# Kernel optimization log

Hardware: AMD Instinct MI355X
Metric: run time of the kernel (lower is better)

## Reference

```python
import jax, jax.numpy as jnp
import numpy as np

B, N, D, H = 8, 2048, 128, 4
DH = D // H
EPS_LN = 1e-5


def setup_inputs() -> dict:
    key = jax.random.key(0)
    ks = jax.random.split(key, 9)
    x = jax.random.normal(ks[0], (B, N, D), dtype=jnp.float32)
    u = jax.random.uniform(ks[1], (N, N), dtype=jnp.float32)
    adj = jnp.where(u > 0.5, u, 0.0)
    adj = adj.at[jnp.arange(N), jnp.arange(N)].set(1.0)
    W = jax.random.normal(ks[2], (D, D), dtype=jnp.float32) * (1.0 / np.sqrt(D))
    a_src = jax.random.normal(ks[3], (H, DH), dtype=jnp.float32) * 0.02
    a_dst = jax.random.normal(ks[4], (H, DH), dtype=jnp.float32) * 0.02
    Wo = jax.random.normal(ks[5], (D, D), dtype=jnp.float32) * (1.0 / np.sqrt(D))
    bo = jnp.zeros((D,), dtype=jnp.float32)
    gamma = jnp.ones((D,), dtype=jnp.float32)
    beta = jnp.zeros((D,), dtype=jnp.float32)
    return {"x": x, "adj_static": adj, "W": W, "a_src": a_src, "a_dst": a_dst,
            "Wo": Wo, "bo": bo, "gamma": gamma, "beta": beta}


def reference(x, adj_static, W, a_src, a_dst, Wo, bo, gamma, beta):
    # h: (B, H, N, DH)
    h = (x @ W.T).reshape(B, N, H, DH).transpose(0, 2, 1, 3)
    src = jnp.einsum('bhnd,hd->bhn', h, a_src)  # (B, H, N)
    dst = jnp.einsum('bhnd,hd->bhn', h, a_dst)  # (B, H, N)
    e = jax.nn.leaky_relu(src[..., :, None] + dst[..., None, :], 0.2)  # (B,H,N,N)
    logA = jnp.log(jnp.clip(adj_static, 1e-8))[None, None]
    mask = (adj_static > 0)[None, None]
    e = jnp.where(mask, e + logA, -jnp.inf)
    attn = jax.nn.softmax(e, axis=-1)  # dropout is identity in eval mode
    out = attn @ h  # (B, H, N, DH)
    out = out.transpose(0, 2, 1, 3).reshape(B, N, D)
    out = out @ Wo.T + bo
    y = x + out
    mu = jnp.mean(y, axis=-1, keepdims=True)
    var = jnp.mean(jnp.square(y - mu), axis=-1, keepdims=True)
    return (y - mu) * jax.lax.rsqrt(var + EPS_LN) * gamma + beta
```

## Files before the change

### kernel.cpp

```cpp
#include <hip/hip_runtime.h>

typedef short bf16x8 __attribute__((ext_vector_type(8)));
typedef float f32x4  __attribute__((ext_vector_type(4)));
typedef float f32x2  __attribute__((ext_vector_type(2)));
typedef int   i32x4  __attribute__((ext_vector_type(4)));
typedef unsigned int u32x2 __attribute__((ext_vector_type(2)));

#define DEV static __device__ __forceinline__
#define LOG2E 1.4426950408889634f

DEV float bfu_to_f(unsigned short s) { return __builtin_bit_cast(float, (unsigned int)s << 16); }
DEV unsigned short f_to_bf(float f) {
  unsigned int u = __builtin_bit_cast(unsigned int, f);
  u += 0x7fffu + ((u >> 16) & 1u);
  return (unsigned short)(u >> 16);
}
DEV unsigned int pack_bf_rne(float lo, float hi) {
  return (unsigned int)f_to_bf(lo) | ((unsigned int)f_to_bf(hi) << 16);
}
DEV float fplo(int u) { return __builtin_bit_cast(float, (unsigned int)u << 16); }
DEV float fphi(int u) { return __builtin_bit_cast(float, (unsigned int)u & 0xffff0000u); }
DEV float nexp2(float x) {
#if __has_builtin(__builtin_amdgcn_exp2f)
  return __builtin_amdgcn_exp2f(x);
#else
  return exp2f(x);
#endif
}
template<bool HI> DEV unsigned int pk_fp8(float a, float b, unsigned int old) {
  return __builtin_amdgcn_cvt_pk_fp8_f32(a, b, old, HI);
}
template<int W> DEV f32x2 upk_fp8(unsigned int w) {
  auto r = __builtin_amdgcn_cvt_pk_f32_fp8(w, W);
  f32x2 o; o[0] = r[0]; o[1] = r[1]; return o;
}

DEV bool detect_f32(const void* adj) { return ((const float*)adj)[0] == 1.0f; }

template<bool F32> DEV float ldS(const void* p, size_t i) {
  if constexpr (F32) return ((const float*)p)[i];
  else               return bfu_to_f(((const unsigned short*)p)[i]);
}
template<bool F32> DEV void ld8f(const void* p, size_t i, float* o) {
  if constexpr (F32) {
    const float* f = (const float*)p + i;
    f32x4 a = *(const f32x4*)f, b = *(const f32x4*)(f + 4);
    o[0]=a[0]; o[1]=a[1]; o[2]=a[2]; o[3]=a[3];
    o[4]=b[0]; o[5]=b[1]; o[6]=b[2]; o[7]=b[3];
  } else {
    i32x4 w = *(const i32x4*)((const unsigned short*)p + i);
#pragma unroll
    for (int k = 0; k < 4; ++k) {
      unsigned int u = (unsigned int)w[k];
      o[2*k]   = __builtin_bit_cast(float, u << 16);
      o[2*k+1] = __builtin_bit_cast(float, u & 0xffff0000u);
    }
  }
}
template<bool F32> DEV bf16x8 ldfrag(const void* p, size_t i) {
  if constexpr (F32) {
    float o[8]; ld8f<true>(p, i, o);
    union { bf16x8 v; unsigned short u[8]; } r;
#pragma unroll
    for (int k = 0; k < 8; ++k) r.u[k] = f_to_bf(o[k]);
    return r.v;
  } else {
    return __builtin_bit_cast(bf16x8, *(const i32x4*)((const unsigned short*)p + i));
  }
}

__global__ __launch_bounds__(256) void k_prep(const void* __restrict__ adj,
                                              unsigned char* __restrict__ adjf) {
  const size_t i0 = ((size_t)blockIdx.x * 256 + threadIdx.x) * 8;
  u32x2 o;
  if (detect_f32(adj)) {
    const float* a = (const float*)adj + i0;
    f32x4 v0 = *(const f32x4*)a, v1 = *(const f32x4*)(a + 4);
    o[0] = pk_fp8<true>(v0[2], v0[3], pk_fp8<false>(v0[0], v0[1], 0u));
    o[1] = pk_fp8<true>(v1[2], v1[3], pk_fp8<false>(v1[0], v1[1], 0u));
  } else {
    i32x4 w = *(const i32x4*)((const unsigned short*)adj + i0);
    float f[8];
#pragma unroll
    for (int k = 0; k < 4; ++k) {
      unsigned int u = (unsigned int)w[k];
      f[2*k]   = __builtin_bit_cast(float, u << 16);
      f[2*k+1] = __builtin_bit_cast(float, u & 0xffff0000u);
    }
    o[0] = pk_fp8<true>(f[2], f[3], pk_fp8<false>(f[0], f[1], 0u));
    o[1] = pk_fp8<true>(f[6], f[7], pk_fp8<false>(f[4], f[5], 0u));
  }
  *(u32x2*)(adjf + i0) = o;
}

template<bool F32> DEV void k_h_body(const void* __restrict__ x, const void* __restrict__ W,
                                     unsigned char* __restrict__ hT,
                                     unsigned short (&t_s)[16][136]) {
  const int tid = threadIdx.x, lane = tid & 63, wave = tid >> 6;
  const int nt = blockIdx.x >> 3, ct = blockIdx.x & 7;
  const int m = lane & 15, q = lane >> 4;
  bf16x8 wf[4];
#pragma unroll
  for (int k = 0; k < 4; ++k)
    wf[k] = ldfrag<F32>(W, (size_t)(ct * 16 + m) * 128 + q * 8 + k * 32);
#pragma unroll
  for (int s = 0; s < 2; ++s) {
    const int nsub = wave * 2 + s;
    const size_t xr = (size_t)(nt * 128 + nsub * 16 + m) * 128 + q * 8;
    f32x4 acc = {0.f, 0.f, 0.f, 0.f};
#pragma unroll
    for (int k = 0; k < 4; ++k)
      acc = __builtin_amdgcn_mfma_f32_16x16x32_bf16(ldfrag<F32>(x, xr + k * 32), wf[k],
                                                    acc, 0, 0, 0);
    u32x2 w2; w2[0] = pack_bf_rne(acc[0], acc[1]); w2[1] = pack_bf_rne(acc[2], acc[3]);
    *(u32x2*)&t_s[m][nsub * 16 + q * 4] = w2;
  }
  __syncthreads();
  const int row = tid >> 4, c8 = tid & 15;
  const int chg = ct * 16 + row, hh = chg >> 5, dloc = chg & 31;
  const int ng = nt * 128 + c8 * 8, b = ng >> 11, nl = ng & 2047;
  i32x4 v = *(const i32x4*)&t_s[row][c8 * 8];
  float f[8];
#pragma unroll
  for (int k = 0; k < 4; ++k) {
    unsigned int u = (unsigned int)v[k];
    f[2*k]   = __builtin_bit_cast(float, u << 16);
    f[2*k+1] = __builtin_bit_cast(float, u & 0xffff0000u);
  }
  u32x2 o;
  o[0] = pk_fp8<true>(f[2], f[3], pk_fp8<false>(f[0], f[1], 0u));
  o[1] = pk_fp8<true>(f[6], f[7], pk_fp8<false>(f[4], f[5], 0u));
  *(u32x2*)(hT + ((size_t)((b * 4 + hh) * 32 + dloc)) * 2048 + nl) = o;
}
__global__ __launch_bounds__(256) void k_h(const void* x, const void* W,
                                           unsigned char* hT, const void* adj) {
  __shared__ __align__(16) unsigned short t_s[16][136];
  if (detect_f32(adj)) k_h_body<true>(x, W, hT, t_s); else k_h_body<false>(x, W, hT, t_s);
}

template<bool F32> DEV void k_sd_body(const unsigned char* __restrict__ hT,
                                      const void* __restrict__ a_src, const void* __restrict__ a_dst,
                                      float* __restrict__ rv, unsigned int* __restrict__ fhv) {
  const int t = blockIdx.x * 256 + threadIdx.x;
  const int n = t & 2047, bh = t >> 11, hh = bh & 3;
  const unsigned char* col = hT + (size_t)bh * 32 * 2048 + n;
  float s = 0.f, d = 0.f;
#pragma unroll
  for (int dd = 0; dd < 32; ++dd) {
    const float v = __builtin_amdgcn_cvt_f32_fp8((int)col[(size_t)dd * 2048], 0);
    s += v * ldS<F32>(a_src, hh * 32 + dd);
    d += v * ldS<F32>(a_dst, hh * 32 + dd);
  }
  rv[t] = nexp2(-0.8f * LOG2E * s);
  const float F = nexp2(LOG2E * d);
  const float H = nexp2(0.2f * LOG2E * d);
  fhv[t] = pack_bf_rne(F, H);
}
__global__ __launch_bounds__(256) void k_sd(const unsigned char* hT, const void* a_src,
                                            const void* a_dst, float* rv, unsigned int* fhv,
                                            const void* adj) {
  if (detect_f32(adj)) k_sd_body<true>(hT, a_src, a_dst, rv, fhv);
  else                 k_sd_body<false>(hT, a_src, a_dst, rv, fhv);
}

struct SmemAttn {
  unsigned char adj[2][64][136];
  unsigned char vt[2][32][136];
  unsigned int  fh[2][128];
};

__global__ __launch_bounds__(256, 4) void k_attn(const unsigned char* __restrict__ adjf,
                                                 const unsigned char* __restrict__ hT,
                                                 const float* __restrict__ rv,
                                                 const unsigned int* __restrict__ fhv,
                                                 unsigned short* __restrict__ ao) {
  __shared__ __align__(16) SmemAttn sm;
  const int tid = threadIdx.x, lane = tid & 63, wave = tid >> 6;
  const int bh = blockIdx.x & 31, iblk = blockIdx.x >> 5;
  const int b = bh >> 2, hh = bh & 3;
  const int m = lane & 15, q = lane >> 4;
  const int i0 = iblk * 64;
  const int jqb = wave * 32 + q * 8;

  const int ar = tid >> 2, ac = (tid & 3) * 32;
  const int vr = tid >> 3, vc = (tid & 7) * 16;
  const bool fstg = tid < 32;

  const unsigned char* ap = adjf + (size_t)(i0 + ar) * 2048 + ac;
  const unsigned char* vp = hT + ((size_t)bh * 32 + vr) * 2048 + vc;
  const unsigned int*  fp = fhv + (size_t)bh * 2048 + tid * 4;

  i32x4 arr0, arr1, vrr, frr;

  arr0 = *(const i32x4*)(ap);
  arr1 = *(const i32x4*)(ap + 16);
  vrr  = *(const i32x4*)vp;
  if (fstg) frr = *(const i32x4*)fp;
  *(i32x4*)&sm.adj[0][ar][ac]      = arr0;
  *(i32x4*)&sm.adj[0][ar][ac + 16] = arr1;
  *(i32x4*)&sm.vt[0][vr][vc] = vrr;
  if (fstg) *(i32x4*)&sm.fh[0][tid * 4] = frr;
  __syncthreads();

  float Riv[4];
#pragma unroll
  for (int it = 0; it < 4; ++it)
    Riv[it] = rv[bh * 2048 + i0 + it * 16 + m];

  f32x4 accA[4], accB[4], accD[4];
#pragma unroll
  for (int it = 0; it < 4; ++it) {
    accA[it] = f32x4{0.f,0.f,0.f,0.f};
    accB[it] = f32x4{0.f,0.f,0.f,0.f};
    accD[it] = f32x4{0.f,0.f,0.f,0.f};
  }
  const long Aones = 0x3838383838383838L;

#pragma unroll 2
  for (int c = 0; c < 16; ++c) {
    const int cb = c & 1;
    if (c < 15) {
      const int o = (c + 1) * 128;
      arr0 = *(const i32x4*)(ap + o);
      arr1 = *(const i32x4*)(ap + o + 16);
      vrr  = *(const i32x4*)(vp + o);
      if (fstg) frr = *(const i32x4*)(fp + o);
    }
    const long A0 = *(const long*)&sm.vt[cb][m][jqb];
    const long A1 = *(const long*)&sm.vt[cb][16 + m][jqb];
    const i32x4 u0 = *(const i32x4*)&sm.fh[cb][jqb];
    const i32x4 u1 = *(const i32x4*)&sm.fh[cb][jqb + 4];
    f32x2 F0 = {fplo(u0[0]), fplo(u0[1])}, H0 = {fphi(u0[0]), fphi(u0[1])};
    f32x2 F1 = {fplo(u0[2]), fplo(u0[3])}, H1 = {fphi(u0[2]), fphi(u0[3])};
    f32x2 F2 = {fplo(u1[0]), fplo(u1[1])}, H2 = {fphi(u1[0]), fphi(u1[1])};
    f32x2 F3 = {fplo(u1[2]), fplo(u1[3])}, H3 = {fphi(u1[2]), fphi(u1[3])};
#pragma unroll
    for (int it = 0; it < 4; ++it) {
      const int il = it * 16 + m;
      const u32x2 aw = *(const u32x2*)&sm.adj[cb][il][jqb];
      f32x2 av0 = upk_fp8<0>(aw[0]), av1 = upk_fp8<1>(aw[0]);
      f32x2 av2 = upk_fp8<0>(aw[1]), av3 = upk_fp8<1>(aw[1]);
      const f32x2 Ri2 = {Riv[it], Riv[it]};
      f32x2 w0 = __builtin_elementwise_max(F0, Ri2 * H0);
      f32x2 w1 = __builtin_elementwise_max(F1, Ri2 * H1);
      f32x2 w2 = __builtin_elementwise_max(F2, Ri2 * H2);
      f32x2 w3 = __builtin_elementwise_max(F3, Ri2 * H3);
      f32x2 pv0 = av0 * w0, pv1 = av1 * w1, pv2 = av2 * w2, pv3 = av3 * w3;
      u32x2 bp;
      bp[0] = pk_fp8<true>(pv1[0], pv1[1], pk_fp8<false>(pv0[0], pv0[1], 0u));
      bp[1] = pk_fp8<true>(pv3[0], pv3[1], pk_fp8<false>(pv2[0], pv2[1], 0u));
      const long B = __builtin_bit_cast(long, bp);
      accA[it] = __builtin_amdgcn_mfma_f32_16x16x32_fp8_fp8(A0,    B, accA[it], 0, 0, 0);
      accB[it] = __builtin_amdgcn_mfma_f32_16x16x32_fp8_fp8(A1,    B, accB[it], 0, 0, 0);
      accD[it] = __builtin_amdgcn_mfma_f32_16x16x32_fp8_fp8(Aones, B, accD[it], 0, 0, 0);
    }
    if (c < 15) {
      const int nb = cb ^ 1;
      *(i32x4*)&sm.adj[nb][ar][ac]      = arr0;
      *(i32x4*)&sm.adj[nb][ar][ac + 16] = arr1;
      *(i32x4*)&sm.vt[nb][vr][vc] = vrr;
      if (fstg) *(i32x4*)&sm.fh[nb][tid * 4] = frr;
    }
    __syncthreads();
  }

  float* red = (float*)&sm;
  if (wave == 1 || wave == 3) {
    const int reg = (wave >> 1) * 3072;
#pragma unroll
    for (int it = 0; it < 4; ++it) {
      const int base = reg + (it * 64 + lane) * 12;
      *(f32x4*)&red[base]     = accA[it];
      *(f32x4*)&red[base + 4] = accB[it];
      red[base + 8] = accD[it][0];
    }
  }
  __syncthreads();
  if (wave == 0 || wave == 2) {
    const int reg = (wave >> 1) * 3072;
#pragma unroll
    for (int it = 0; it < 4; ++it) {
      const int base = reg + (it * 64 + lane) * 12;
      accA[it] += *(const f32x4*)&red[base];
      accB[it] += *(const f32x4*)&red[base + 4];
      accD[it][0] += red[base + 8];
    }
  }
  __syncthreads();
  if (wave == 2) {
#pragma unroll
    for (int it = 0; it < 4; ++it) {
      const int base = (it * 64 + lane) * 12;
      *(f32x4*)&red[base]     = accA[it];
      *(f32x4*)&red[base + 4] = accB[it];
      red[base + 8] = accD[it][0];
    }
  }
  __syncthreads();
  if (wave == 0) {
#pragma unroll
    for (int it = 0; it < 4; ++it) {
      const int base = (it * 64 + lane) * 12;
      const f32x4 a0 = accA[it] + *(const f32x4*)&red[base];
      const f32x4 a1 = accB[it] + *(const f32x4*)&red[base + 4];
      const float den = accD[it][0] + red[base + 8];
      const float inv = 1.f / fmaxf(den, 1e-20f);
      const int il = it * 16 + m;
      unsigned short* op = ao + ((size_t)(b * 2048) + i0 + il) * 128 + hh * 32 + q * 4;
      u32x2 w0, w1;
      w0[0] = pack_bf_rne(a0[0] * inv, a0[1] * inv);
      w0[1] = pack_bf_rne(a0[2] * inv, a0[3] * inv);
      w1[0] = pack_bf_rne(a1[0] * inv, a1[1] * inv);
      w1[1] = pack_bf_rne(a1[2] * inv, a1[3] * inv);
      *(u32x2*)op        = w0;
      *(u32x2*)(op + 16) = w1;
    }
  }
}

template<bool F32> DEV void k_out_body(const unsigned short* __restrict__ ao,
                                       const void* __restrict__ Wo, const void* __restrict__ bo,
                                       const void* __restrict__ x, const void* __restrict__ gamma,
                                       const void* __restrict__ beta, void* __restrict__ out,
                                       float (&y_s)[16][132]) {
  const int tid = threadIdx.x, lane = tid & 63, wave = tid >> 6;
  const int m = lane & 15, q = lane >> 4;
  const int rbase = blockIdx.x * 16;
  bf16x8 af[4];
#pragma unroll
  for (int k = 0; k < 4; ++k)
    af[k] = ldfrag<false>(ao, ((size_t)(rbase + m)) * 128 + q * 8 + k * 32);
  f32x4 acc[2] = {{0.f,0.f,0.f,0.f},{0.f,0.f,0.f,0.f}};
#pragma unroll
  for (int ct = 0; ct < 2; ++ct) {
    const size_t wrow = (size_t)(wave * 32 + ct * 16 + m) * 128 + q * 8;
#pragma unroll
    for (int k = 0; k < 4; ++k)
      acc[ct] = __builtin_amdgcn_mfma_f32_16x16x32_bf16(af[k], ldfrag<F32>(Wo, wrow + k * 32),
                                                        acc[ct], 0, 0, 0);
  }
#pragma unroll
  for (int ct = 0; ct < 2; ++ct) {
    const int c = wave * 32 + ct * 16 + m;
    const float bov = ldS<F32>(bo, c);
#pragma unroll
    for (int r = 0; r < 4; ++r) {
      const int row = q * 4 + r;
      y_s[row][c] = acc[ct][r] + bov + ldS<F32>(x, (size_t)(rbase + row) * 128 + c);
    }
  }
  __syncthreads();
  const int r = tid >> 4, c16 = tid & 15;
  float vals[8], sum = 0.f, sq = 0.f;
#pragma unroll
  for (int k = 0; k < 8; ++k) {
    const float v = y_s[r][c16 * 8 + k];
    vals[k] = v; sum += v; sq += v * v;
  }
#pragma unroll
  for (int msk = 1; msk < 16; msk <<= 1) {
    sum += __shfl_xor(sum, msk, 16);
    sq  += __shfl_xor(sq,  msk, 16);
  }
  const float mu  = sum * (1.f / 128.f);
  const float var = fmaxf(sq * (1.f / 128.f) - mu * mu, 0.f);
  const float rstd = rsqrtf(var + 1e-5f);
  float o[8];
#pragma unroll
  for (int k = 0; k < 8; ++k) {
    const int c = c16 * 8 + k;
    o[k] = (vals[k] - mu) * rstd * ldS<F32>(gamma, c) + ldS<F32>(beta, c);
  }
  const size_t obase = (size_t)(rbase + r) * 128 + c16 * 8;
  if constexpr (F32) {
    float* op = (float*)out + obase;
    f32x4 w0 = {o[0],o[1],o[2],o[3]}, w1 = {o[4],o[5],o[6],o[7]};
    *(f32x4*)op = w0; *(f32x4*)(op + 4) = w1;
  } else {
    union { unsigned short u[8]; i32x4 v; } ob;
#pragma unroll
    for (int k = 0; k < 8; ++k) ob.u[k] = f_to_bf(o[k]);
    *(i32x4*)((unsigned short*)out + obase) = ob.v;
  }
}
__global__ __launch_bounds__(256) void k_out(const unsigned short* ao, const void* Wo,
                                             const void* bo, const void* x, const void* gamma,
                                             const void* beta, void* out, const void* adj) {
  __shared__ __align__(16) float y_s[16][132];
  if (detect_f32(adj)) k_out_body<true>(ao, Wo, bo, x, gamma, beta, out, y_s);
  else                 k_out_body<false>(ao, Wo, bo, x, gamma, beta, out, y_s);
}

extern "C" void kernel_launch(void* const* d_in, const int* in_sizes, int n_in,
                              void* d_out, int out_size, void* d_ws, size_t ws_size,
                              hipStream_t stream) {
  const void* x     = d_in[0];
  const void* adj   = d_in[1];
  const void* W     = d_in[2];
  const void* a_src = d_in[3];
  const void* a_dst = d_in[4];
  const void* Wo    = d_in[5];
  const void* bo    = d_in[6];
  const void* gamma = d_in[7];
  const void* beta  = d_in[8];

  char* ws = (char*)d_ws;
  unsigned char*  hT_ws  = (unsigned char*)ws;
  unsigned short* ao_ws  = (unsigned short*)(ws + 2097152);
  float*          rv_ws  = (float*)(ws + 6291456);
  unsigned int*   fh_ws  = (unsigned int*)(ws + 6553600);
  unsigned char*  adjf   = (unsigned char*)(ws + 6815744);

  k_prep<<<2048, 256, 0, stream>>>(adj, adjf);
  k_h   <<<1024, 256, 0, stream>>>(x, W, hT_ws, adj);
  k_sd  <<<256,  256, 0, stream>>>(hT_ws, a_src, a_dst, rv_ws, fh_ws, adj);
  k_attn<<<1024, 256, 0, stream>>>(adjf, hT_ws, rv_ws, fh_ws, ao_ws);
  k_out <<<1024, 256, 0, stream>>>(ao_ws, Wo, bo, x, gamma, beta, d_out, adj);
}
```

Measured before the change: 147.2 us.

## Switch attention pipeline from fp8 to fp16 with packed fp16 weight math

Intermediate adjacency, transposed h, and the attention weight factors are stored in fp16 instead of fp8/bf16. The attention kernel computes the weights with packed fp16 vector max/mul and uses fp16 MFMA, replacing the per-element fp8 unpack/repack conversions. The row tile shrinks from 64 to 32 and the grid doubles to keep shared memory in bounds. The cost is twice the global and LDS traffic for adj and h and half the MFMA throughput of fp8, in exchange for fewer conversion instructions and better accuracy.

```diff
diff --git a/kernel.cpp b/kernel.cpp
--- a/kernel.cpp
+++ b/kernel.cpp
@@ -1,6 +1,8 @@
 #include <hip/hip_runtime.h>
 
 typedef short bf16x8 __attribute__((ext_vector_type(8)));
+typedef _Float16 f16x8 __attribute__((ext_vector_type(8)));
+typedef _Float16 f16x2 __attribute__((ext_vector_type(2)));
 typedef float f32x4  __attribute__((ext_vector_type(4)));
 typedef float f32x2  __attribute__((ext_vector_type(2)));
 typedef int   i32x4  __attribute__((ext_vector_type(4)));
@@ -18,21 +20,19 @@
 DEV unsigned int pack_bf_rne(float lo, float hi) {
   return (unsigned int)f_to_bf(lo) | ((unsigned int)f_to_bf(hi) << 16);
 }
-DEV float fplo(int u) { return __builtin_bit_cast(float, (unsigned int)u << 16); }
-DEV float fphi(int u) { return __builtin_bit_cast(float, (unsigned int)u & 0xffff0000u); }
+DEV unsigned int pk_f16(float a, float b) {
+  auto h = __builtin_amdgcn_cvt_pkrtz(a, b);
+  return __builtin_bit_cast(unsigned int, h);
+}
+DEV unsigned short f_to_f16(float a) {
+  return __builtin_bit_cast(unsigned short, (_Float16)a);
+}
 DEV float nexp2(float x) {
 #if __has_builtin(__builtin_amdgcn_exp2f)
   return __builtin_amdgcn_exp2f(x);
 #else
   return exp2f(x);
 #endif
-}
-template<bool HI> DEV unsigned int pk_fp8(float a, float b, unsigned int old) {
-  return __builtin_amdgcn_cvt_pk_fp8_f32(a, b, old, HI);
-}
-template<int W> DEV f32x2 upk_fp8(unsigned int w) {
-  auto r = __builtin_amdgcn_cvt_pk_f32_fp8(w, W);
-  f32x2 o; o[0] = r[0]; o[1] = r[1]; return o;
 }
 
 DEV bool detect_f32(const void* adj) { return ((const float*)adj)[0] == 1.0f; }
@@ -70,31 +70,22 @@
 }
 
 __global__ __launch_bounds__(256) void k_prep(const void* __restrict__ adj,
-                                              unsigned char* __restrict__ adjf) {
+                                              unsigned short* __restrict__ adjh) {
   const size_t i0 = ((size_t)blockIdx.x * 256 + threadIdx.x) * 8;
-  u32x2 o;
+  float f[8];
   if (detect_f32(adj)) {
-    const float* a = (const float*)adj + i0;
-    f32x4 v0 = *(const f32x4*)a, v1 = *(const f32x4*)(a + 4);
-    o[0] = pk_fp8<true>(v0[2], v0[3], pk_fp8<false>(v0[0], v0[1], 0u));
-    o[1] = pk_fp8<true>(v1[2], v1[3], pk_fp8<false>(v1[0], v1[1], 0u));
+    ld8f<true>(adj, i0, f);
   } else {
-    i32x4 w = *(const i32x4*)((const unsigned short*)adj + i0);
-    float f[8];
-#pragma unroll
-    for (int k = 0; k < 4; ++k) {
-      unsigned int u = (unsigned int)w[k];
-      f[2*k]   = __builtin_bit_cast(float, u << 16);
-      f[2*k+1] = __builtin_bit_cast(float, u & 0xffff0000u);
-    }
-    o[0] = pk_fp8<true>(f[2], f[3], pk_fp8<false>(f[0], f[1], 0u));
-    o[1] = pk_fp8<true>(f[6], f[7], pk_fp8<false>(f[4], f[5], 0u));
-  }
-  *(u32x2*)(adjf + i0) = o;
+    ld8f<false>(adj, i0, f);
+  }
+  i32x4 o;
+#pragma unroll
+  for (int k = 0; k < 4; ++k) o[k] = (int)pk_f16(f[2*k], f[2*k+1]);
+  *(i32x4*)(adjh + i0) = o;
 }
 
 template<bool F32> DEV void k_h_body(const void* __restrict__ x, const void* __restrict__ W,
-                                     unsigned char* __restrict__ hT,
+                                     unsigned short* __restrict__ hT,
                                      unsigned short (&t_s)[16][136]) {
   const int tid = threadIdx.x, lane = tid & 63, wave = tid >> 6;
   const int nt = blockIdx.x >> 3, ct = blockIdx.x & 7;
@@ -127,148 +118,150 @@
     f[2*k]   = __builtin_bit_cast(float, u << 16);
     f[2*k+1] = __builtin_bit_cast(float, u & 0xffff0000u);
   }
-  u32x2 o;
-  o[0] = pk_fp8<true>(f[2], f[3], pk_fp8<false>(f[0], f[1], 0u));
-  o[1] = pk_fp8<true>(f[6], f[7], pk_fp8<false>(f[4], f[5], 0u));
-  *(u32x2*)(hT + ((size_t)((b * 4 + hh) * 32 + dloc)) * 2048 + nl) = o;
+  i32x4 o;
+#pragma unroll
+  for (int k = 0; k < 4; ++k) o[k] = (int)pk_f16(f[2*k], f[2*k+1]);
+  *(i32x4*)(hT + ((size_t)((b * 4 + hh) * 32 + dloc)) * 2048 + nl) = o;
 }
 __global__ __launch_bounds__(256) void k_h(const void* x, const void* W,
-                                           unsigned char* hT, const void* adj) {
+                                           unsigned short* hT, const void* adj) {
   __shared__ __align__(16) unsigned short t_s[16][136];
   if (detect_f32(adj)) k_h_body<true>(x, W, hT, t_s); else k_h_body<false>(x, W, hT, t_s);
 }
 
-template<bool F32> DEV void k_sd_body(const unsigned char* __restrict__ hT,
+template<bool F32> DEV void k_sd_body(const unsigned short* __restrict__ hT,
                                       const void* __restrict__ a_src, const void* __restrict__ a_dst,
-                                      float* __restrict__ rv, unsigned int* __restrict__ fhv) {
+                                      unsigned int* __restrict__ rvh,
+                                      unsigned short* __restrict__ Fh,
+                                      unsigned short* __restrict__ Hh) {
   const int t = blockIdx.x * 256 + threadIdx.x;
   const int n = t & 2047, bh = t >> 11, hh = bh & 3;
-  const unsigned char* col = hT + (size_t)bh * 32 * 2048 + n;
+  const unsigned short* col = hT + (size_t)bh * 32 * 2048 + n;
   float s = 0.f, d = 0.f;
 #pragma unroll
   for (int dd = 0; dd < 32; ++dd) {
-    const float v = __builtin_amdgcn_cvt_f32_fp8((int)col[(size_t)dd * 2048], 0);
+    const float v = (float)__builtin_bit_cast(_Float16, col[(size_t)dd * 2048]);
     s += v * ldS<F32>(a_src, hh * 32 + dd);
     d += v * ldS<F32>(a_dst, hh * 32 + dd);
   }
-  rv[t] = nexp2(-0.8f * LOG2E * s);
+  const float R = nexp2(-0.8f * LOG2E * s);
   const float F = nexp2(LOG2E * d);
   const float H = nexp2(0.2f * LOG2E * d);
-  fhv[t] = pack_bf_rne(F, H);
-}
-__global__ __launch_bounds__(256) void k_sd(const unsigned char* hT, const void* a_src,
-                                            const void* a_dst, float* rv, unsigned int* fhv,
+  rvh[t] = pk_f16(R, R);
+  Fh[t] = f_to_f16(F);
+  Hh[t] = f_to_f16(H);
+}
+__global__ __launch_bounds__(256) void k_sd(const unsigned short* hT, const void* a_src,
+                                            const void* a_dst, unsigned int* rvh,
+                                            unsigned short* Fh, unsigned short* Hh,
                                             const void* adj) {
-  if (detect_f32(adj)) k_sd_body<true>(hT, a_src, a_dst, rv, fhv);
-  else                 k_sd_body<false>(hT, a_src, a_dst, rv, fhv);
+  if (detect_f32(adj)) k_sd_body<true>(hT, a_src, a_dst, rvh, Fh, Hh);
+  else                 k_sd_body<false>(hT, a_src, a_dst, rvh, Fh, Hh);
 }
 
 struct SmemAttn {
-  unsigned char adj[2][64][136];
-  unsigned char vt[2][32][136];
-  unsigned int  fh[2][128];
+  unsigned char adj[2][32][272];
+  unsigned char vt[2][32][272];
+  unsigned short Fs[2][128];
+  unsigned short Hs[2][128];
 };
 
-__global__ __launch_bounds__(256, 4) void k_attn(const unsigned char* __restrict__ adjf,
-                                                 const unsigned char* __restrict__ hT,
-                                                 const float* __restrict__ rv,
-                                                 const unsigned int* __restrict__ fhv,
+__global__ __launch_bounds__(256, 4) void k_attn(const unsigned short* __restrict__ adjh,
+                                                 const unsigned short* __restrict__ hTh,
+                                                 const unsigned int* __restrict__ rvh,
+                                                 const unsigned short* __restrict__ Fh,
+                                                 const unsigned short* __restrict__ Hh,
                                                  unsigned short* __restrict__ ao) {
   __shared__ __align__(16) SmemAttn sm;
   const int tid = threadIdx.x, lane = tid & 63, wave = tid >> 6;
   const int bh = blockIdx.x & 31, iblk = blockIdx.x >> 5;
   const int b = bh >> 2, hh = bh & 3;
   const int m = lane & 15, q = lane >> 4;
-  const int i0 = iblk * 64;
-  const int jqb = wave * 32 + q * 8;
-
-  const int ar = tid >> 2, ac = (tid & 3) * 32;
-  const int vr = tid >> 3, vc = (tid & 7) * 16;
+  const int i0 = iblk * 32;
+
+  const int ar = tid >> 3, ac = (tid & 7) * 32;
   const bool fstg = tid < 32;
 
-  const unsigned char* ap = adjf + (size_t)(i0 + ar) * 2048 + ac;
-  const unsigned char* vp = hT + ((size_t)bh * 32 + vr) * 2048 + vc;
-  const unsigned int*  fp = fhv + (size_t)bh * 2048 + tid * 4;
-
-  i32x4 arr0, arr1, vrr, frr;
-
-  arr0 = *(const i32x4*)(ap);
-  arr1 = *(const i32x4*)(ap + 16);
-  vrr  = *(const i32x4*)vp;
+  const unsigned char* ap = (const unsigned char*)adjh + (size_t)(i0 + ar) * 4096 + ac;
+  const unsigned char* vp = (const unsigned char*)hTh + ((size_t)bh * 32 + ar) * 4096 + ac;
+  const unsigned short* fp = (tid < 16 ? Fh : Hh) + (size_t)bh * 2048 + (tid & 15) * 8;
+
+  i32x4 a0r, a1r, v0r, v1r, frr;
+
+  a0r = *(const i32x4*)(ap);      a1r = *(const i32x4*)(ap + 16);
+  v0r = *(const i32x4*)(vp);      v1r = *(const i32x4*)(vp + 16);
   if (fstg) frr = *(const i32x4*)fp;
-  *(i32x4*)&sm.adj[0][ar][ac]      = arr0;
-  *(i32x4*)&sm.adj[0][ar][ac + 16] = arr1;
-  *(i32x4*)&sm.vt[0][vr][vc] = vrr;
-  if (fstg) *(i32x4*)&sm.fh[0][tid * 4] = frr;
-  __syncthreads();
-
-  float Riv[4];
-#pragma unroll
-  for (int it = 0; it < 4; ++it)
-    Riv[it] = rv[bh * 2048 + i0 + it * 16 + m];
-
-  f32x4 accA[4], accB[4], accD[4];
-#pragma unroll
-  for (int it = 0; it < 4; ++it) {
+  *(i32x4*)&sm.adj[0][ar][ac]      = a0r;
+  *(i32x4*)&sm.adj[0][ar][ac + 16] = a1r;
+  *(i32x4*)&sm.vt[0][ar][ac]       = v0r;
+  *(i32x4*)&sm.vt[0][ar][ac + 16]  = v1r;
+  if (fstg) {
+    unsigned short* d = (tid < 16) ? &sm.Fs[0][(tid & 15) * 8] : &sm.Hs[0][(tid & 15) * 8];
+    *(i32x4*)d = frr;
+  }
+  __syncthreads();
+
+  unsigned int riw[2];
+#pragma unroll
+  for (int it = 0; it < 2; ++it)
+    riw[it] = rvh[bh * 2048 + i0 + it * 16 + m];
+
+  f32x4 accA[2], accB[2], accD[2];
+#pragma unroll
+  for (int it = 0; it < 2; ++it) {
     accA[it] = f32x4{0.f,0.f,0.f,0.f};
     accB[it] = f32x4{0.f,0.f,0.f,0.f};
     accD[it] = f32x4{0.f,0.f,0.f,0.f};
   }
-  const long Aones = 0x3838383838383838L;
+  const i32x4 onev = {0x3C003C00, 0x3C003C00, 0x3C003C00, 0x3C003C00};
+  const f16x8 ONE8 = __builtin_bit_cast(f16x8, onev);
+
+  const int jq = wave * 32 + q * 8;
+  const int jb = jq * 2;
 
 #pragma unroll 2
   for (int c = 0; c < 16; ++c) {
     const int cb = c & 1;
     if (c < 15) {
-      const int o = (c + 1) * 128;
-      arr0 = *(const i32x4*)(ap + o);
-      arr1 = *(const i32x4*)(ap + o + 16);
-      vrr  = *(const i32x4*)(vp + o);
-      if (fstg) frr = *(const i32x4*)(fp + o);
-    }
-    const long A0 = *(const long*)&sm.vt[cb][m][jqb];
-    const long A1 = *(const long*)&sm.vt[cb][16 + m][jqb];
-    const i32x4 u0 = *(const i32x4*)&sm.fh[cb][jqb];
-    const i32x4 u1 = *(const i32x4*)&sm.fh[cb][jqb + 4];
-    f32x2 F0 = {fplo(u0[0]), fplo(u0[1])}, H0 = {fphi(u0[0]), fphi(u0[1])};
-    f32x2 F1 = {fplo(u0[2]), fplo(u0[3])}, H1 = {fphi(u0[2]), fphi(u0[3])};
-    f32x2 F2 = {fplo(u1[0]), fplo(u1[1])}, H2 = {fphi(u1[0]), fphi(u1[1])};
-    f32x2 F3 = {fplo(u1[2]), fplo(u1[3])}, H3 = {fphi(u1[2]), fphi(u1[3])};
-#pragma unroll
-    for (int it = 0; it < 4; ++it) {
-      const int il = it * 16 + m;
-      const u32x2 aw = *(const u32x2*)&sm.adj[cb][il][jqb];
-      f32x2 av0 = upk_fp8<0>(aw[0]), av1 = upk_fp8<1>(aw[0]);
-      f32x2 av2 = upk_fp8<0>(aw[1]), av3 = upk_fp8<1>(aw[1]);
-      const f32x2 Ri2 = {Riv[it], Riv[it]};
-      f32x2 w0 = __builtin_elementwise_max(F0, Ri2 * H0);
-      f32x2 w1 = __builtin_elementwise_max(F1, Ri2 * H1);
-      f32x2 w2 = __builtin_elementwise_max(F2, Ri2 * H2);
-      f32x2 w3 = __builtin_elementwise_max(F3, Ri2 * H3);
-      f32x2 pv0 = av0 * w0, pv1 = av1 * w1, pv2 = av2 * w2, pv3 = av3 * w3;
-      u32x2 bp;
-      bp[0] = pk_fp8<true>(pv1[0], pv1[1], pk_fp8<false>(pv0[0], pv0[1], 0u));
-      bp[1] = pk_fp8<true>(pv3[0], pv3[1], pk_fp8<false>(pv2[0], pv2[1], 0u));
-      const long B = __builtin_bit_cast(long, bp);
-      accA[it] = __builtin_amdgcn_mfma_f32_16x16x32_fp8_fp8(A0,    B, accA[it], 0, 0, 0);
-      accB[it] = __builtin_amdgcn_mfma_f32_16x16x32_fp8_fp8(A1,    B, accB[it], 0, 0, 0);
-      accD[it] = __builtin_amdgcn_mfma_f32_16x16x32_fp8_fp8(Aones, B, accD[it], 0, 0, 0);
+      const int o = (c + 1) * 256;
+      a0r = *(const i32x4*)(ap + o);      a1r = *(const i32x4*)(ap + o + 16);
+      v0r = *(const i32x4*)(vp + o);      v1r = *(const i32x4*)(vp + o + 16);
+      if (fstg) frr = *(const i32x4*)(fp + (c + 1) * 128);
+    }
+    const f16x8 A0 = *(const f16x8*)&sm.vt[cb][m][jb];
+    const f16x8 A1 = *(const f16x8*)&sm.vt[cb][16 + m][jb];
+    const f16x8 F8 = *(const f16x8*)&sm.Fs[cb][jq];
+    const f16x8 H8 = *(const f16x8*)&sm.Hs[cb][jq];
+#pragma unroll
+    for (int it = 0; it < 2; ++it) {
+      const f16x8 aw = *(const f16x8*)&sm.adj[cb][it * 16 + m][jb];
+      const i32x4 rb = {(int)riw[it], (int)riw[it], (int)riw[it], (int)riw[it]};
+      const f16x8 R8 = __builtin_bit_cast(f16x8, rb);
+      const f16x8 w8 = __builtin_elementwise_max(F8, R8 * H8);
+      const f16x8 p8 = aw * w8;
+      accA[it] = __builtin_amdgcn_mfma_f32_16x16x32_f16(A0,   p8, accA[it], 0, 0, 0);
+      accB[it] = __builtin_amdgcn_mfma_f32_16x16x32_f16(A1,   p8, accB[it], 0, 0, 0);
+      accD[it] = __builtin_amdgcn_mfma_f32_16x16x32_f16(ONE8, p8, accD[it], 0, 0, 0);
     }
     if (c < 15) {
       const int nb = cb ^ 1;
-      *(i32x4*)&sm.adj[nb][ar][ac]      = arr0;
-      *(i32x4*)&sm.adj[nb][ar][ac + 16] = arr1;
-      *(i32x4*)&sm.vt[nb][vr][vc] = vrr;
-      if (fstg) *(i32x4*)&sm.fh[nb][tid * 4] = frr;
+      *(i32x4*)&sm.adj[nb][ar][ac]      = a0r;
+      *(i32x4*)&sm.adj[nb][ar][ac + 16] = a1r;
+      *(i32x4*)&sm.vt[nb][ar][ac]       = v0r;
+      *(i32x4*)&sm.vt[nb][ar][ac + 16]  = v1r;
+      if (fstg) {
+        unsigned short* d = (tid < 16) ? &sm.Fs[nb][(tid & 15) * 8] : &sm.Hs[nb][(tid & 15) * 8];
+        *(i32x4*)d = frr;
+      }
     }
     __syncthreads();
   }
 
   float* red = (float*)&sm;
   if (wave == 1 || wave == 3) {
-    const int reg = (wave >> 1) * 3072;
-#pragma unroll
-    for (int it = 0; it < 4; ++it) {
+    const int reg = (wave >> 1) * 1536;
+#pragma unroll
+    for (int it = 0; it < 2; ++it) {
       const int base = reg + (it * 64 + lane) * 12;
       *(f32x4*)&red[base]     = accA[it];
       *(f32x4*)&red[base + 4] = accB[it];
@@ -277,9 +270,9 @@
   }
   __syncthreads();
   if (wave == 0 || wave == 2) {
-    const int reg = (wave >> 1) * 3072;
-#pragma unroll
-    for (int it = 0; it < 4; ++it) {
+    const int reg = (wave >> 1) * 1536;
+#pragma unroll
+    for (int it = 0; it < 2; ++it) {
       const int base = reg + (it * 64 + lane) * 12;
       accA[it] += *(const f32x4*)&red[base];
       accB[it] += *(const f32x4*)&red[base + 4];
@@ -289,7 +282,7 @@
   __syncthreads();
   if (wave == 2) {
 #pragma unroll
-    for (int it = 0; it < 4; ++it) {
+    for (int it = 0; it < 2; ++it) {
       const int base = (it * 64 + lane) * 12;
       *(f32x4*)&red[base]     = accA[it];
       *(f32x4*)&red[base + 4] = accB[it];
@@ -299,7 +292,7 @@
   __syncthreads();
   if (wave == 0) {
 #pragma unroll
-    for (int it = 0; it < 4; ++it) {
+    for (int it = 0; it < 2; ++it) {
       const int base = (it * 64 + lane) * 12;
       const f32x4 a0 = accA[it] + *(const f32x4*)&red[base];
       const f32x4 a1 = accB[it] + *(const f32x4*)&red[base + 4];
@@ -405,15 +398,16 @@
   const void* beta  = d_in[8];
 
   char* ws = (char*)d_ws;
-  unsigned char*  hT_ws  = (unsigned char*)ws;
-  unsigned short* ao_ws  = (unsigned short*)(ws + 2097152);
-  float*          rv_ws  = (float*)(ws + 6291456);
-  unsigned int*   fh_ws  = (unsigned int*)(ws + 6553600);
-  unsigned char*  adjf   = (unsigned char*)(ws + 6815744);
-
-  k_prep<<<2048, 256, 0, stream>>>(adj, adjf);
-  k_h   <<<1024, 256, 0, stream>>>(x, W, hT_ws, adj);
-  k_sd  <<<256,  256, 0, stream>>>(hT_ws, a_src, a_dst, rv_ws, fh_ws, adj);
-  k_attn<<<1024, 256, 0, stream>>>(adjf, hT_ws, rv_ws, fh_ws, ao_ws);
+  unsigned short* hTh   = (unsigned short*)ws;
+  unsigned short* ao_ws = (unsigned short*)(ws + 4194304);
+  unsigned int*   rvh   = (unsigned int*)(ws + 8388608);
+  unsigned short* Fh    = (unsigned short*)(ws + 8650752);
+  unsigned short* Hh    = (unsigned short*)(ws + 8781824);
+  unsigned short* adjh  = (unsigned short*)(ws + 8912896);
+
+  k_prep<<<2048, 256, 0, stream>>>(adj, adjh);
+  k_h   <<<1024, 256, 0, stream>>>(x, W, hTh, adj);
+  k_sd  <<<256,  256, 0, stream>>>(hTh, a_src, a_dst, rvh, Fh, Hh, adj);
+  k_attn<<<2048, 256, 0, stream>>>(adjh, hTh, rvh, Fh, Hh, ao_ws);
   k_out <<<1024, 256, 0, stream>>>(ao_ws, Wo, bo, x, gamma, beta, d_out, adj);
 }
```

Result: no change. 148.8 us (+1.1%).
